# Optimization experiments

Measured on AMD Instinct MI355X. Metric: run time of the kernel, lower is better.

The kernel has to match this reference:

```python
import jax, jax.numpy as jnp
import numpy as np

N_NODES = 4194304  # 2**22
LEVELS = 10
COARSE = 8192
RANK = 2
NNZ = 8388608


def _interp_linear(u, N):
    """torch F.interpolate(mode='linear', align_corners=False) along axis 1. u: (B,M,R) -> (B,N,R)."""
    M = u.shape[1]
    pos = (jnp.arange(N, dtype=jnp.float32) + 0.5) * (M / N) - 0.5
    pos = jnp.clip(pos, 0.0, M - 1)
    i0 = jnp.floor(pos).astype(jnp.int32)
    i1 = jnp.minimum(i0 + 1, M - 1)
    w = (pos - i0.astype(jnp.float32))[None, :, None]
    return u[:, i0] * (1.0 - w) + u[:, i1] * w


def _apply_hodlr(diag, u_factors, v_factors, x):
    B, N, _ = x.shape
    y = diag * x
    L = u_factors.shape[0]
    for lvl in range(L):
        num_splits = 2 ** (lvl + 1)
        bs = N // num_splits
        if bs == 0:
            continue
        uc, vc = u_factors[lvl], v_factors[lvl]
        u_full = _interp_linear(uc, N) if uc.shape[1] != N else uc
        v_full = _interp_linear(vc, N) if vc.shape[1] != N else vc
        P = num_splits // 2
        valid = P * 2 * bs
        xv = x[:, :valid].reshape(B, P, 2, bs, 1)
        uv = u_full[:, :valid].reshape(B, P, 2, bs, -1)
        vv = v_full[:, :valid].reshape(B, P, 2, bs, -1)
        xL, xR = xv[:, :, 0], xv[:, :, 1]
        uL, uR = uv[:, :, 0], uv[:, :, 1]
        vL, vR = vv[:, :, 0], vv[:, :, 1]
        xRp = jnp.einsum('bpkr,bpko->bpro', vR, xR)  # (B,P,R,1)
        xLp = jnp.einsum('bpkr,bpko->bpro', vL, xL)
        yL = jnp.einsum('bpkr,bpro->bpko', uL, xRp)  # (B,P,bs,1)
        yR = jnp.einsum('bpkr,bpro->bpko', uR, xLp)
        upd = jnp.stack([yL, yR], axis=2).reshape(B, valid, 1)
        if valid < N:
            upd = jnp.pad(upd, ((0, 0), (0, N - valid), (0, 0)))
        y = y + upd
    return y


def setup_inputs() -> dict:
    key = jax.random.key(0)
    ks = jax.random.split(key, 6)
    diag = jax.random.uniform(ks[0], (1, N_NODES, 1), dtype=jnp.float32)
    u_factors = jax.random.normal(ks[1], (LEVELS, 1, COARSE, RANK), dtype=jnp.float32)
    v_factors = jax.random.normal(ks[2], (LEVELS, 1, COARSE, RANK), dtype=jnp.float32)
    A_values = jax.random.normal(ks[3], (NNZ,), dtype=jnp.float32)
    z = jax.random.normal(ks[4], (1, N_NODES, 1), dtype=jnp.float32)
    A_indices = jax.random.randint(ks[5], (2, NNZ), 0, N_NODES, dtype=jnp.int64) if jax.config.jax_enable_x64 else jax.random.randint(ks[5], (2, NNZ), 0, N_NODES, dtype=jnp.int32)
    return {"diag": diag, "u_factors": u_factors, "v_factors": v_factors,
            "A_values": A_values, "z": z, "A_indices": A_indices, "num_nodes": N_NODES}


def reference(diag, u_factors, v_factors, A_values, z, A_indices, num_nodes):
    N = num_nodes
    w = _apply_hodlr(diag, u_factors, v_factors, z)          # (1,N,1)
    w_flat = w.reshape(N)
    rows, cols = A_indices[0], A_indices[1]
    y_flat = jax.ops.segment_sum(A_values * w_flat[cols], rows, num_segments=N)
    y = y_flat.reshape(1, N, 1)
    loss = jnp.mean((y - z) ** 2)
    return loss
```

## Files before the change

### kernel.cpp

```cpp
#include <hip/hip_runtime.h>

#define N_NODES 4194304
#define LEVELS  10
#define COARSE  8192
#define NNZ_E   8388608
#define NB      256
#define NSUB    512
#define RB_SZ   16384
#define EPB     8192
#define CAP_SUB 17920u

typedef int          v4i __attribute__((ext_vector_type(4)));
typedef float        v4f __attribute__((ext_vector_type(4)));
typedef unsigned int v4u __attribute__((ext_vector_type(4)));
typedef unsigned int v2u __attribute__((ext_vector_type(2)));

static __device__ __forceinline__ unsigned short f2bf(float x) {
    unsigned u = __float_as_uint(x);
    return (unsigned short)((u + 0x7FFFu + ((u >> 16) & 1u)) >> 16);
}
static __device__ __forceinline__ float bf2f(unsigned short h) {
    return __uint_as_float((unsigned)h << 16);
}

__global__ __launch_bounds__(512) void kA(const float* __restrict__ z,
                                          float2* __restrict__ M,
                                          float* __restrict__ S,
                                          float* __restrict__ out,
                                          const int* __restrict__ rows,
                                          const int* __restrict__ cols,
                                          const float* __restrict__ vals,
                                          unsigned* __restrict__ subCtr,
                                          v2u* __restrict__ rowBinned) {
    int b = blockIdx.x, t = threadIdx.x;
    if (b < 2048) {
        if (b == 0) {
            for (int i = t; i < 2046 * 2; i += 512) S[i] = 0.f;
            if (t == 0) out[0] = 0.f;
        }
        int lane = t & 63, wave = t >> 6;
        int chunk = b * 8 + wave;
        int base = chunk * 256 + lane * 4;
        float4 zv = *(const float4*)(z + base);
        float a0 = 0.f, a1 = 0.f;
        const float* zp = (const float*)&zv;
#pragma unroll
        for (int j = 0; j < 4; ++j) {
            float p = ((float)(base + j) + 0.5f) * (1.0f / 512.0f) - 0.5f;
            p = fminf(fmaxf(p, 0.0f), (float)(COARSE - 1));
            float f = p - floorf(p);
            a0 += zp[j] * (1.0f - f);
            a1 += zp[j] * f;
        }
#pragma unroll
        for (int off = 32; off >= 1; off >>= 1) {
            a0 += __shfl_xor(a0, off, 64);
            a1 += __shfl_xor(a1, off, 64);
        }
        if (lane == 0) M[chunk] = make_float2(a0, a1);
    } else {
        __shared__ v2u sortedP[EPB];
        __shared__ unsigned cur[NSUB], gb[NSUB];
        __shared__ unsigned wsum[8], wbase[8];
        int blk = b - 2048;
        int base = blk * EPB;
        v4i r[4], c[4];
        v4f v[4];
#pragma unroll
        for (int j = 0; j < 4; ++j) {
            int e = base + j * 2048 + t * 4;
            r[j] = __builtin_nontemporal_load((const v4i*)(rows + e));
            c[j] = __builtin_nontemporal_load((const v4i*)(cols + e));
            v[j] = __builtin_nontemporal_load((const v4f*)(vals + e));
        }
        cur[t] = 0u;
        __syncthreads();
#pragma unroll
        for (int j = 0; j < 4; ++j) {
            const int* rp = (const int*)&r[j];
            const int* cp = (const int*)&c[j];
#pragma unroll
            for (int kk = 0; kk < 4; ++kk) {
                unsigned sub = (((unsigned)rp[kk] >> 14) << 1) | ((unsigned)cp[kk] >> 21);
                atomicAdd(&cur[sub], 1u);
            }
        }
        __syncthreads();
        unsigned lv = cur[t];
        unsigned lincl = lv;
#pragma unroll
        for (int off = 1; off < 64; off <<= 1) {
            unsigned n = __shfl_up(lincl, off, 64);
            if ((t & 63) >= off) lincl += n;
        }
        if ((t & 63) == 63) wsum[t >> 6] = lincl;
        __syncthreads();
        if (t == 0) {
            unsigned a = 0;
            for (int i = 0; i < 8; ++i) { wbase[i] = a; a += wsum[i]; }
        }
        __syncthreads();
        {
            unsigned lexcl = wbase[t >> 6] + lincl - lv;
            gb[t] = (unsigned)t * CAP_SUB + atomicAdd(&subCtr[t], lv) - lexcl;
            cur[t] = lexcl;
        }
        __syncthreads();
#pragma unroll
        for (int j = 0; j < 4; ++j) {
            const int* rp = (const int*)&r[j];
            const int* cp = (const int*)&c[j];
            const float* vp = (const float*)&v[j];
#pragma unroll
            for (int kk = 0; kk < 4; ++kk) {
                unsigned row = (unsigned)rp[kk], col = (unsigned)cp[kk];
                unsigned sub = ((row >> 14) << 1) | (col >> 21);
                unsigned rl = row & 16383u;
                v2u ent;
                ent.x = col | ((rl & 0x3FFu) << 22);
                ent.y = (rl >> 10) | (sub << 4) | ((unsigned)f2bf(vp[kk]) << 16);
                unsigned i = atomicAdd(&cur[sub], 1u);
                sortedP[i] = ent;
            }
        }
        __syncthreads();
#pragma unroll
        for (int k = 0; k < 16; ++k) {
            int i = k * 512 + t;
            v2u e = sortedP[i];
            unsigned bkt = (e.y >> 4) & 0x1FFu;
            __builtin_nontemporal_store(e, rowBinned + gb[bkt] + i);
        }
    }
}

__global__ __launch_bounds__(256) void kB(const float2* __restrict__ M,
                                          const float* __restrict__ V,
                                          float* __restrict__ S) {
    int b = blockIdx.x, t = threadIdx.x;
    int lvl = b >> 3, slice = b & 7;
    const float2* Vl = (const float2*)(V + lvl * COARSE * 2);
    float s0 = 0.f, s1 = 0.f;
    int c0 = slice * 2048 + t * 8;
#pragma unroll
    for (int cc = 0; cc < 8; ++cc) {
        int c = c0 + cc;
        float2 m = M[c];
        int k = (c > 0) ? ((c - 1) >> 1) : 0;
        int kp = min(k + 1, COARSE - 1);
        float2 vk = Vl[k], vkp = Vl[kp];
        s0 += vk.x * m.x + vkp.x * m.y;
        s1 += vk.y * m.x + vkp.y * m.y;
    }
    int gw = min(1 << (10 - lvl), 64);
    for (int sh = gw >> 1; sh >= 1; sh >>= 1) {
        s0 += __shfl_xor(s0, sh, 64);
        s1 += __shfl_xor(s1, sh, 64);
    }
    if ((t & (gw - 1)) == 0) {
        int bb = c0 >> (13 - lvl);
        int soff = (2 << lvl) - 2;
        unsafeAtomicAdd(&S[(soff + bb) * 2 + 0], s0);
        unsafeAtomicAdd(&S[(soff + bb) * 2 + 1], s1);
    }
}

__global__ __launch_bounds__(512) void kCw(const float* __restrict__ diag,
                                           const float* __restrict__ z,
                                           const float* __restrict__ S,
                                           const float* __restrict__ U,
                                           unsigned short* __restrict__ wb) {
    int b = blockIdx.x, t = threadIdx.x;
    int tid = b * 512 + t;
    int base = tid * 4;
    int c = base >> 8;
    int k = (c > 0) ? ((c - 1) >> 1) : 0;
    int kp = min(k + 1, COARSE - 1);
    float g0 = 0.f, g1 = 0.f;
#pragma unroll
    for (int lvl = 0; lvl < LEVELS; ++lvl) {
        int sib = (c >> (13 - lvl)) ^ 1;
        int soff = (2 << lvl) - 2;
        float2 s2 = ((const float2*)S)[soff + sib];
        const float2* Ul = (const float2*)(U + lvl * COARSE * 2);
        float2 uk = Ul[k], ukp = Ul[kp];
        g0 += uk.x * s2.x + uk.y * s2.y;
        g1 += ukp.x * s2.x + ukp.y * s2.y;
    }
    float4 d4 = *(const float4*)(diag + base);
    float4 z4 = *(const float4*)(z + base);
    const float* dp = (const float*)&d4;
    const float* zp = (const float*)&z4;
    ushort4 h4;
    unsigned short* hp = (unsigned short*)&h4;
#pragma unroll
    for (int j = 0; j < 4; ++j) {
        float p = ((float)(base + j) + 0.5f) * (1.0f / 512.0f) - 0.5f;
        p = fminf(fmaxf(p, 0.0f), (float)(COARSE - 1));
        float f = p - floorf(p);
        hp[j] = f2bf(dp[j] * zp[j] + (g0 + f * (g1 - g0)));
    }
    *(ushort4*)(wb + base) = h4;
}

__global__ __launch_bounds__(1024) void kE(const v2u* __restrict__ rowBinned,
                                           const unsigned* __restrict__ subCtr,
                                           const unsigned short* __restrict__ wb,
                                           const float* __restrict__ z,
                                           float* __restrict__ out) {
    __shared__ float acc[RB_SZ];
    __shared__ float red[16];
    int b = blockIdx.x, t = threadIdx.x;

    for (int i = t; i < RB_SZ / 4; i += 1024) ((float4*)acc)[i] = make_float4(0.f, 0.f, 0.f, 0.f);
    __syncthreads();

#pragma unroll 1
    for (int h = 0; h < 2; ++h) {
        int s = b * 2 + h;
        unsigned n = subCtr[s];
        const v2u* seg = rowBinned + (size_t)s * CAP_SUB;
        unsigned i = t;
        for (; i + 7u * 1024u < n; i += 8u * 1024u) {
            v2u ev[8];
#pragma unroll
            for (int k = 0; k < 8; ++k)
                ev[k] = __builtin_nontemporal_load(seg + i + (unsigned)k * 1024u);
            unsigned short wv[8];
#pragma unroll
            for (int k = 0; k < 8; ++k)
                wv[k] = wb[ev[k].x & 0x3FFFFFu];
#pragma unroll
            for (int k = 0; k < 8; ++k) {
                unsigned rl = (ev[k].x >> 22) | ((ev[k].y & 0xFu) << 10);
                float p = bf2f((unsigned short)(ev[k].y >> 16)) * bf2f(wv[k]);
                atomicAdd(&acc[rl], p);
            }
        }
        for (; i < n; i += 1024u) {
            v2u e = __builtin_nontemporal_load(seg + i);
            unsigned rl = (e.x >> 22) | ((e.y & 0xFu) << 10);
            float p = bf2f((unsigned short)(e.y >> 16)) * bf2f(wb[e.x & 0x3FFFFFu]);
            atomicAdd(&acc[rl], p);
        }
    }
    __syncthreads();

    float part = 0.f;
    int gbase = b * RB_SZ;
    for (int k = t; k < RB_SZ; k += 1024) {
        float d = acc[k] - z[gbase + k];
        part += d * d;
    }
#pragma unroll
    for (int off = 32; off >= 1; off >>= 1) part += __shfl_xor(part, off, 64);
    if ((t & 63) == 0) red[t >> 6] = part;
    __syncthreads();
    if (t == 0) {
        float s = 0.f;
        for (int k = 0; k < 16; ++k) s += red[k];
        unsafeAtomicAdd(out, s * (1.0f / (float)N_NODES));
    }
}

extern "C" void kernel_launch(void* const* d_in, const int* in_sizes, int n_in,
                              void* d_out, int out_size, void* d_ws, size_t ws_size,
                              hipStream_t stream) {
    const float* diag  = (const float*)d_in[0];
    const float* U     = (const float*)d_in[1];
    const float* V     = (const float*)d_in[2];
    const float* Avals = (const float*)d_in[3];
    const float* z     = (const float*)d_in[4];
    const int*   Aidx  = (const int*)d_in[5];
    const int* rows = Aidx;
    const int* cols = Aidx + NNZ_E;

    char* ws = (char*)d_ws;
    size_t off = 0;
    unsigned short* wb  = (unsigned short*)(ws + off); off += (size_t)N_NODES * 2;
    v2u* rowBinned      = (v2u*)(ws + off);            off += (size_t)NSUB * CAP_SUB * 8;
    unsigned* subCtr    = (unsigned*)(ws + off);       off += NSUB * 4;
    float2* M           = (float2*)(ws + off);         off += (size_t)(N_NODES / 256) * 8;
    float* S            = (float*)(ws + off);          off += 16384;

    hipMemsetAsync(subCtr, 0, NSUB * 4, stream);
    kA<<<3072, 512, 0, stream>>>(z, M, S, (float*)d_out, rows, cols, Avals, subCtr, rowBinned);
    kB<<<80, 256, 0, stream>>>(M, V, S);
    kCw<<<2048, 512, 0, stream>>>(diag, z, S, U, wb);
    kE<<<NB, 1024, 0, stream>>>(rowBinned, subCtr, wb, z, (float*)d_out);
}
```

Measured before the change: 295.4 us.

## Gather w before binning and store packed 4-byte products per row segment

The edge binning moves out of the first kernel into a new kernel that runs after w is computed. It gathers w[col] directly from the unsorted edges and multiplies by the value, then bins a single 32-bit entry holding a 13-bit local row and a 19-bit truncated float product into 512 row segments of 8192. The final kernel only streams these packed products and does shared-memory atomic adds, with no random w gather. This halves the bytes written and read for the binned array, but the bin write can no longer overlap the HODLR stage, and the product keeps only 19 bits.

```diff
diff --git a/kernel.cpp b/kernel.cpp
--- a/kernel.cpp
+++ b/kernel.cpp
@@ -4,16 +4,14 @@
 #define LEVELS  10
 #define COARSE  8192
 #define NNZ_E   8388608
-#define NB      256
-#define NSUB    512
-#define RB_SZ   16384
+#define NSEG    512
+#define RB_SZ   8192
 #define EPB     8192
-#define CAP_SUB 17920u
+#define CAP_SEG 18432u
 
 typedef int          v4i __attribute__((ext_vector_type(4)));
 typedef float        v4f __attribute__((ext_vector_type(4)));
 typedef unsigned int v4u __attribute__((ext_vector_type(4)));
-typedef unsigned int v2u __attribute__((ext_vector_type(2)));
 
 static __device__ __forceinline__ unsigned short f2bf(float x) {
     unsigned u = __float_as_uint(x);
@@ -23,115 +21,35 @@
     return __uint_as_float((unsigned)h << 16);
 }
 
-__global__ __launch_bounds__(512) void kA(const float* __restrict__ z,
+__global__ __launch_bounds__(512) void k1(const float* __restrict__ z,
                                           float2* __restrict__ M,
                                           float* __restrict__ S,
-                                          float* __restrict__ out,
-                                          const int* __restrict__ rows,
-                                          const int* __restrict__ cols,
-                                          const float* __restrict__ vals,
-                                          unsigned* __restrict__ subCtr,
-                                          v2u* __restrict__ rowBinned) {
-    int b = blockIdx.x, t = threadIdx.x;
-    if (b < 2048) {
-        if (b == 0) {
-            for (int i = t; i < 2046 * 2; i += 512) S[i] = 0.f;
-            if (t == 0) out[0] = 0.f;
-        }
-        int lane = t & 63, wave = t >> 6;
-        int chunk = b * 8 + wave;
-        int base = chunk * 256 + lane * 4;
-        float4 zv = *(const float4*)(z + base);
-        float a0 = 0.f, a1 = 0.f;
-        const float* zp = (const float*)&zv;
-#pragma unroll
-        for (int j = 0; j < 4; ++j) {
-            float p = ((float)(base + j) + 0.5f) * (1.0f / 512.0f) - 0.5f;
-            p = fminf(fmaxf(p, 0.0f), (float)(COARSE - 1));
-            float f = p - floorf(p);
-            a0 += zp[j] * (1.0f - f);
-            a1 += zp[j] * f;
-        }
-#pragma unroll
-        for (int off = 32; off >= 1; off >>= 1) {
-            a0 += __shfl_xor(a0, off, 64);
-            a1 += __shfl_xor(a1, off, 64);
-        }
-        if (lane == 0) M[chunk] = make_float2(a0, a1);
-    } else {
-        __shared__ v2u sortedP[EPB];
-        __shared__ unsigned cur[NSUB], gb[NSUB];
-        __shared__ unsigned wsum[8], wbase[8];
-        int blk = b - 2048;
-        int base = blk * EPB;
-        v4i r[4], c[4];
-        v4f v[4];
-#pragma unroll
-        for (int j = 0; j < 4; ++j) {
-            int e = base + j * 2048 + t * 4;
-            r[j] = __builtin_nontemporal_load((const v4i*)(rows + e));
-            c[j] = __builtin_nontemporal_load((const v4i*)(cols + e));
-            v[j] = __builtin_nontemporal_load((const v4f*)(vals + e));
-        }
-        cur[t] = 0u;
-        __syncthreads();
-#pragma unroll
-        for (int j = 0; j < 4; ++j) {
-            const int* rp = (const int*)&r[j];
-            const int* cp = (const int*)&c[j];
-#pragma unroll
-            for (int kk = 0; kk < 4; ++kk) {
-                unsigned sub = (((unsigned)rp[kk] >> 14) << 1) | ((unsigned)cp[kk] >> 21);
-                atomicAdd(&cur[sub], 1u);
-            }
-        }
-        __syncthreads();
-        unsigned lv = cur[t];
-        unsigned lincl = lv;
-#pragma unroll
-        for (int off = 1; off < 64; off <<= 1) {
-            unsigned n = __shfl_up(lincl, off, 64);
-            if ((t & 63) >= off) lincl += n;
-        }
-        if ((t & 63) == 63) wsum[t >> 6] = lincl;
-        __syncthreads();
-        if (t == 0) {
-            unsigned a = 0;
-            for (int i = 0; i < 8; ++i) { wbase[i] = a; a += wsum[i]; }
-        }
-        __syncthreads();
-        {
-            unsigned lexcl = wbase[t >> 6] + lincl - lv;
-            gb[t] = (unsigned)t * CAP_SUB + atomicAdd(&subCtr[t], lv) - lexcl;
-            cur[t] = lexcl;
-        }
-        __syncthreads();
-#pragma unroll
-        for (int j = 0; j < 4; ++j) {
-            const int* rp = (const int*)&r[j];
-            const int* cp = (const int*)&c[j];
-            const float* vp = (const float*)&v[j];
-#pragma unroll
-            for (int kk = 0; kk < 4; ++kk) {
-                unsigned row = (unsigned)rp[kk], col = (unsigned)cp[kk];
-                unsigned sub = ((row >> 14) << 1) | (col >> 21);
-                unsigned rl = row & 16383u;
-                v2u ent;
-                ent.x = col | ((rl & 0x3FFu) << 22);
-                ent.y = (rl >> 10) | (sub << 4) | ((unsigned)f2bf(vp[kk]) << 16);
-                unsigned i = atomicAdd(&cur[sub], 1u);
-                sortedP[i] = ent;
-            }
-        }
-        __syncthreads();
-#pragma unroll
-        for (int k = 0; k < 16; ++k) {
-            int i = k * 512 + t;
-            v2u e = sortedP[i];
-            unsigned bkt = (e.y >> 4) & 0x1FFu;
-            __builtin_nontemporal_store(e, rowBinned + gb[bkt] + i);
-        }
-    }
+                                          float* __restrict__ out) {
+    int b = blockIdx.x, t = threadIdx.x;
+    if (b == 0) {
+        for (int i = t; i < 2046 * 2; i += 512) S[i] = 0.f;
+        if (t == 0) out[0] = 0.f;
+    }
+    int lane = t & 63, wave = t >> 6;
+    int chunk = b * 8 + wave;
+    int base = chunk * 256 + lane * 4;
+    float4 zv = *(const float4*)(z + base);
+    float a0 = 0.f, a1 = 0.f;
+    const float* zp = (const float*)&zv;
+#pragma unroll
+    for (int j = 0; j < 4; ++j) {
+        float p = ((float)(base + j) + 0.5f) * (1.0f / 512.0f) - 0.5f;
+        p = fminf(fmaxf(p, 0.0f), (float)(COARSE - 1));
+        float f = p - floorf(p);
+        a0 += zp[j] * (1.0f - f);
+        a1 += zp[j] * f;
+    }
+#pragma unroll
+    for (int off = 32; off >= 1; off >>= 1) {
+        a0 += __shfl_xor(a0, off, 64);
+        a1 += __shfl_xor(a1, off, 64);
+    }
+    if (lane == 0) M[chunk] = make_float2(a0, a1);
 }
 
 __global__ __launch_bounds__(256) void kB(const float2* __restrict__ M,
@@ -203,9 +121,95 @@
     *(ushort4*)(wb + base) = h4;
 }
 
-__global__ __launch_bounds__(1024) void kE(const v2u* __restrict__ rowBinned,
-                                           const unsigned* __restrict__ subCtr,
+__global__ __launch_bounds__(1024) void k2(const int* __restrict__ rows,
+                                           const int* __restrict__ cols,
+                                           const float* __restrict__ vals,
                                            const unsigned short* __restrict__ wb,
+                                           unsigned* __restrict__ segCtr,
+                                           unsigned* __restrict__ binned) {
+    __shared__ unsigned sortedP[EPB];
+    __shared__ unsigned short sortedB[EPB];
+    __shared__ unsigned cur[NSEG], gb[NSEG];
+    __shared__ unsigned wsum[16], wbase[16];
+    int blk = blockIdx.x, t = threadIdx.x;
+    int base = blk * EPB;
+    v4i r[2], c[2];
+    v4f v[2];
+#pragma unroll
+    for (int j = 0; j < 2; ++j) {
+        int e = base + j * 4096 + t * 4;
+        r[j] = __builtin_nontemporal_load((const v4i*)(rows + e));
+        c[j] = __builtin_nontemporal_load((const v4i*)(cols + e));
+        v[j] = __builtin_nontemporal_load((const v4f*)(vals + e));
+    }
+    float wf[8];
+#pragma unroll
+    for (int j = 0; j < 2; ++j) {
+        const int* cp = (const int*)&c[j];
+#pragma unroll
+        for (int kk = 0; kk < 4; ++kk)
+            wf[j * 4 + kk] = bf2f(wb[(unsigned)cp[kk]]);
+    }
+    if (t < NSEG) cur[t] = 0u;
+    __syncthreads();
+#pragma unroll
+    for (int j = 0; j < 2; ++j) {
+        const int* rp = (const int*)&r[j];
+#pragma unroll
+        for (int kk = 0; kk < 4; ++kk)
+            atomicAdd(&cur[(unsigned)rp[kk] >> 13], 1u);
+    }
+    __syncthreads();
+    unsigned lv = 0, lincl = 0;
+    if (t < NSEG) {
+        lv = cur[t];
+        lincl = lv;
+#pragma unroll
+        for (int off = 1; off < 64; off <<= 1) {
+            unsigned n = __shfl_up(lincl, off, 64);
+            if ((t & 63) >= off) lincl += n;
+        }
+        if ((t & 63) == 63) wsum[t >> 6] = lincl;
+    }
+    __syncthreads();
+    if (t == 0) {
+        unsigned a = 0;
+        for (int i = 0; i < 8; ++i) { wbase[i] = a; a += wsum[i]; }
+    }
+    __syncthreads();
+    if (t < NSEG) {
+        unsigned lexcl = wbase[t >> 6] + lincl - lv;
+        gb[t] = (unsigned)t * CAP_SEG + atomicAdd(&segCtr[t], lv) - lexcl;
+        cur[t] = lexcl;
+    }
+    __syncthreads();
+#pragma unroll
+    for (int j = 0; j < 2; ++j) {
+        const int* rp = (const int*)&r[j];
+        const float* vp = (const float*)&v[j];
+#pragma unroll
+        for (int kk = 0; kk < 4; ++kk) {
+            unsigned row = (unsigned)rp[kk];
+            unsigned seg = row >> 13;
+            unsigned rl = row & 8191u;
+            float p = wf[j * 4 + kk] * vp[kk];
+            unsigned pe = ((__float_as_uint(p) + 0x1000u) >> 13) & 0x7FFFFu;
+            unsigned i = atomicAdd(&cur[seg], 1u);
+            sortedP[i] = (rl << 19) | pe;
+            sortedB[i] = (unsigned short)seg;
+        }
+    }
+    __syncthreads();
+#pragma unroll
+    for (int k = 0; k < 8; ++k) {
+        int i = k * 1024 + t;
+        unsigned s = sortedB[i];
+        __builtin_nontemporal_store(sortedP[i], binned + gb[s] + i);
+    }
+}
+
+__global__ __launch_bounds__(1024) void kE(const unsigned* __restrict__ binned,
+                                           const unsigned* __restrict__ segCtr,
                                            const float* __restrict__ z,
                                            float* __restrict__ out) {
     __shared__ float acc[RB_SZ];
@@ -215,34 +219,21 @@
     for (int i = t; i < RB_SZ / 4; i += 1024) ((float4*)acc)[i] = make_float4(0.f, 0.f, 0.f, 0.f);
     __syncthreads();
 
-#pragma unroll 1
-    for (int h = 0; h < 2; ++h) {
-        int s = b * 2 + h;
-        unsigned n = subCtr[s];
-        const v2u* seg = rowBinned + (size_t)s * CAP_SUB;
-        unsigned i = t;
-        for (; i + 7u * 1024u < n; i += 8u * 1024u) {
-            v2u ev[8];
-#pragma unroll
-            for (int k = 0; k < 8; ++k)
-                ev[k] = __builtin_nontemporal_load(seg + i + (unsigned)k * 1024u);
-            unsigned short wv[8];
-#pragma unroll
-            for (int k = 0; k < 8; ++k)
-                wv[k] = wb[ev[k].x & 0x3FFFFFu];
-#pragma unroll
-            for (int k = 0; k < 8; ++k) {
-                unsigned rl = (ev[k].x >> 22) | ((ev[k].y & 0xFu) << 10);
-                float p = bf2f((unsigned short)(ev[k].y >> 16)) * bf2f(wv[k]);
-                atomicAdd(&acc[rl], p);
-            }
-        }
-        for (; i < n; i += 1024u) {
-            v2u e = __builtin_nontemporal_load(seg + i);
-            unsigned rl = (e.x >> 22) | ((e.y & 0xFu) << 10);
-            float p = bf2f((unsigned short)(e.y >> 16)) * bf2f(wb[e.x & 0x3FFFFFu]);
-            atomicAdd(&acc[rl], p);
-        }
+    unsigned n = segCtr[b];
+    const unsigned* seg = binned + (size_t)b * CAP_SEG;
+    unsigned i = t;
+    for (; i + 7u * 1024u < n; i += 8u * 1024u) {
+        unsigned ev[8];
+#pragma unroll
+        for (int k = 0; k < 8; ++k)
+            ev[k] = __builtin_nontemporal_load(seg + i + (unsigned)k * 1024u);
+#pragma unroll
+        for (int k = 0; k < 8; ++k)
+            atomicAdd(&acc[ev[k] >> 19], __uint_as_float((ev[k] & 0x7FFFFu) << 13));
+    }
+    for (; i < n; i += 1024u) {
+        unsigned e = __builtin_nontemporal_load(seg + i);
+        atomicAdd(&acc[e >> 19], __uint_as_float((e & 0x7FFFFu) << 13));
     }
     __syncthreads();
 
@@ -278,14 +269,15 @@
     char* ws = (char*)d_ws;
     size_t off = 0;
     unsigned short* wb  = (unsigned short*)(ws + off); off += (size_t)N_NODES * 2;
-    v2u* rowBinned      = (v2u*)(ws + off);            off += (size_t)NSUB * CAP_SUB * 8;
-    unsigned* subCtr    = (unsigned*)(ws + off);       off += NSUB * 4;
+    unsigned* binned    = (unsigned*)(ws + off);       off += (size_t)NSEG * CAP_SEG * 4;
+    unsigned* segCtr    = (unsigned*)(ws + off);       off += NSEG * 4;
     float2* M           = (float2*)(ws + off);         off += (size_t)(N_NODES / 256) * 8;
     float* S            = (float*)(ws + off);          off += 16384;
 
-    hipMemsetAsync(subCtr, 0, NSUB * 4, stream);
-    kA<<<3072, 512, 0, stream>>>(z, M, S, (float*)d_out, rows, cols, Avals, subCtr, rowBinned);
+    hipMemsetAsync(segCtr, 0, NSEG * 4, stream);
+    k1<<<2048, 512, 0, stream>>>(z, M, S, (float*)d_out);
     kB<<<80, 256, 0, stream>>>(M, V, S);
     kCw<<<2048, 512, 0, stream>>>(diag, z, S, U, wb);
-    kE<<<NB, 1024, 0, stream>>>(rowBinned, subCtr, wb, z, (float*)d_out);
-}
+    k2<<<1024, 1024, 0, stream>>>(rows, cols, Avals, wb, segCtr, binned);
+    kE<<<NSEG, 1024, 0, stream>>>(binned, segCtr, z, (float*)d_out);
+}
```

After: 317.8 us. 7.6% more time.
